# Performance work log

Measured on AMD Instinct MI355X. Metric: run time of the kernel, lower is better.

## Reference

```python
import jax, jax.numpy as jnp
import numpy as np

H = 64  # hidden size


def _lstm(hist, Wih, Whh, bih, bhh):
    # PyTorch single-layer LSTM, gate order [i, f, g, o]; hist: (T, in_dim)
    def step(carry, x):
        h, c = carry
        gates = Wih @ x + bih + Whh @ h + bhh  # (4H,)
        i, f, g, o = jnp.split(gates, 4)
        i, f, o = jax.nn.sigmoid(i), jax.nn.sigmoid(f), jax.nn.sigmoid(o)
        c = f * c + i * jnp.tanh(g)
        h = o * jnp.tanh(c)
        return (h, c), None
    h0 = jnp.zeros((H,), hist.dtype)
    (h, _), _ = jax.lax.scan(step, (h0, h0), hist)
    return h


def setup_inputs() -> dict:
    key = jax.random.key(0)
    ks = jax.random.split(key, 16)
    N, E, P, T = 100000, 3200000, 1000000, 200
    s = 0.05
    return {
        "node_feats": jax.random.normal(ks[0], (N, 2), jnp.float32),
        "edge_feats": jax.random.normal(ks[1], (E, 5), jnp.float32),
        "hist_tokens": jax.random.normal(ks[2], (T, 3), jnp.float32),
        "cand_pairs": jax.random.randint(ks[3], (P, 2), 0, N, jnp.int32),
        "N": N,
        "node_W": jax.random.normal(ks[4], (2, H), jnp.float32) * s,
        "node_b": jax.random.normal(ks[5], (H,), jnp.float32) * s,
        "edge_W": jax.random.normal(ks[6], (5, H), jnp.float32) * s,
        "edge_b": jax.random.normal(ks[7], (H,), jnp.float32) * s,
        "lstm_Wih": jax.random.normal(ks[8], (4 * H, 3), jnp.float32) * s,
        "lstm_Whh": jax.random.normal(ks[9], (4 * H, H), jnp.float32) * s,
        "lstm_bih": jax.random.normal(ks[10], (4 * H,), jnp.float32) * s,
        "lstm_bhh": jax.random.normal(ks[11], (4 * H,), jnp.float32) * s,
        "fuse_W1": jax.random.normal(ks[12], (3 * H + 2, H), jnp.float32) * s,
        "fuse_b1": jax.random.normal(ks[13], (H,), jnp.float32) * s,
        "fuse_W2": jax.random.normal(ks[14], (H, 1), jnp.float32) * s,
        "fuse_b2": jax.random.normal(ks[15], (1,), jnp.float32) * s,
    }


def reference(node_feats, edge_feats, hist_tokens, cand_pairs, N,
              node_W, node_b, edge_W, edge_b,
              lstm_Wih, lstm_Whh, lstm_bih, lstm_bhh,
              fuse_W1, fuse_b1, fuse_W2, fuse_b2):
    # encoder: mean-pooled node / edge MLPs -> (2H,)
    hn = jax.nn.relu(node_feats @ node_W + node_b).mean(0)
    he = jax.nn.relu(edge_feats @ edge_W + edge_b).mean(0)
    z_graph = jnp.concatenate([hn, he])  # (2H,)
    z_hist = _lstm(hist_tokens, lstm_Wih, lstm_Whh, lstm_bih, lstm_bhh)  # (H,)
    P = cand_pairs.shape[0]
    denom = jnp.float32(N - 1) + 1e-9
    cand = cand_pairs.astype(jnp.float32) / denom  # (P, 2)
    ctx = jnp.concatenate([z_graph, z_hist])  # (3H,)
    z = jnp.concatenate([jnp.broadcast_to(ctx, (P, 3 * H)), cand], axis=-1)  # (P, 3H+2)
    scores = jax.nn.relu(z @ fuse_W1 + fuse_b1) @ fuse_W2 + fuse_b2  # (P, 1)
    return scores[:, 0]
```

## Files before the change

kernel.cpp:

```cpp
#include <hip/hip_runtime.h>
#include <math.h>

#define H 64
#define WS_H 0
#define WS_FUSE 64
#define WS_PART 320
#define LOG2E 1.4426950408889634f

__device__ __forceinline__ float fast_sigmoid(float x) {
    float e = exp2f(-LOG2E * x);
    return __builtin_amdgcn_rcpf(1.f + e);
}
__device__ __forceinline__ float fast_tanh(float x) {
    x = fminf(fmaxf(x, -9.f), 9.f);
    float e = exp2f((2.f * LOG2E) * x);
    return (e - 1.f) * __builtin_amdgcn_rcpf(e + 1.f);
}

template<int K>
__device__ void encode_rows2(const float* __restrict__ X, const float* __restrict__ Wg,
                             const float* __restrict__ bias, int nrows,
                             int blk, int nblk, float* __restrict__ out, int tid)
{
    constexpr int TR = 512;
    __shared__ __align__(16) float xs[TR * K];
    int lane = tid & 63;
    int j0 = (tid >> 6) * 16;
    float w[K][16], bi[16], acc[16];
#pragma unroll
    for (int k = 0; k < K; ++k)
#pragma unroll
        for (int jj = 0; jj < 16; ++jj) w[k][jj] = Wg[k * H + j0 + jj];
#pragma unroll
    for (int jj = 0; jj < 16; ++jj) { bi[jj] = bias[j0 + jj]; acc[jj] = 0.f; }

    int ntiles = (nrows + TR - 1) / TR;
    for (int tile = blk; tile < ntiles; tile += nblk) {
        size_t base = (size_t)tile * TR;
        int cnt = nrows - (int)base; if (cnt > TR) cnt = TR;
        int ne = cnt * K;
        __syncthreads();
        const float* Xb = X + base * K;
        int n4 = ne >> 2;
        for (int idx = tid; idx < n4; idx += 256)
            ((float4*)xs)[idx] = ((const float4*)Xb)[idx];
        for (int idx = (n4 << 2) + tid; idx < ne; idx += 256)
            xs[idx] = Xb[idx];
        __syncthreads();
#pragma unroll
        for (int i = 0; i < TR / 64; ++i) {
            int r = i * 64 + lane;
            if (r < cnt) {
                float x[K];
#pragma unroll
                for (int k = 0; k < K; ++k) x[k] = xs[r * K + k];
#pragma unroll
                for (int jj = 0; jj < 16; ++jj) {
                    float t = bi[jj];
#pragma unroll
                    for (int k = 0; k < K; ++k) t = fmaf(x[k], w[k][jj], t);
                    acc[jj] += fmaxf(t, 0.f);
                }
            }
        }
    }
#pragma unroll
    for (int jj = 0; jj < 16; ++jj) {
        float v = acc[jj];
#pragma unroll
        for (int off = 32; off; off >>= 1) v += __shfl_xor(v, off);
        if (lane == jj) out[j0 + jj] = v;
    }
}

__global__ __launch_bounds__(256)
void k_encode_lstm(const float* __restrict__ node_feats,
                   const float* __restrict__ edge_feats,
                   const float* __restrict__ hist,
                   const float* __restrict__ node_W, const float* __restrict__ node_b,
                   const float* __restrict__ edge_W, const float* __restrict__ edge_b,
                   const float* __restrict__ Wih, const float* __restrict__ Whh,
                   const float* __restrict__ bih, const float* __restrict__ bhh,
                   int Nn, int Ne, int T, int eb, int nb,
                   float* __restrict__ ws)
{
    int tid = threadIdx.x;
    int b = blockIdx.x;

    if (b == 0) {
        __builtin_amdgcn_s_setprio(1);
        __shared__ float hcop[4][H];
        __shared__ __align__(16) float4 actx[2][H];
        __shared__ float hist_s[640];
        int w = tid >> 6, j = tid & 63;
        int row = tid;
        float whh[H];
#pragma unroll
        for (int k = 0; k < H; k += 4) {
            float4 v = *(const float4*)(Whh + row * H + k);
            whh[k] = v.x; whh[k+1] = v.y; whh[k+2] = v.z; whh[k+3] = v.w;
        }
        float wih0 = Wih[row*3+0], wih1 = Wih[row*3+1], wih2 = Wih[row*3+2];
        float bsum = bih[row] + bhh[row];
        for (int idx = tid; idx < T * 3; idx += 256) hist_s[idx] = hist[idx];
        hcop[w][j] = 0.f;
        float c = 0.f, h = 0.f;
        __syncthreads();

        for (int t = 0; t < T; ++t) {
            float x0 = hist_s[3*t], x1 = hist_s[3*t+1], x2 = hist_s[3*t+2];
            float g = fmaf(wih0, x0, fmaf(wih1, x1, fmaf(wih2, x2, bsum)));
            float a0 = 0.f, a1 = 0.f, a2 = 0.f, a3 = 0.f;
            const float4* hv = (const float4*)hcop[w];
#pragma unroll
            for (int k4 = 0; k4 < H / 4; ++k4) {
                float4 hh = hv[k4];
                a0 = fmaf(whh[4*k4+0], hh.x, a0);
                a1 = fmaf(whh[4*k4+1], hh.y, a1);
                a2 = fmaf(whh[4*k4+2], hh.z, a2);
                a3 = fmaf(whh[4*k4+3], hh.w, a3);
            }
            g += (a0 + a1) + (a2 + a3);
            float av = (w == 2) ? fast_tanh(g) : fast_sigmoid(g);
            ((float*)&actx[t & 1][j])[w] = av;
            __syncthreads();
            float4 a = actx[t & 1][j];
            c = fmaf(a.y, c, a.x * a.z);
            h = a.w * fast_tanh(c);
            hcop[w][j] = h;
        }
        if (w == 0) ws[WS_H + j] = h;
    } else if (b <= eb) {
        encode_rows2<5>(edge_feats, edge_W, edge_b, Ne, b - 1, eb,
                        ws + WS_PART + (size_t)(b - 1) * H, tid);
    } else {
        encode_rows2<2>(node_feats, node_W, node_b, Nn, b - 1 - eb, nb,
                        ws + WS_PART + (size_t)(eb + (b - 1 - eb)) * H, tid);
    }
}

__global__ __launch_bounds__(1024)
void k_finalize(const float* __restrict__ W1, const float* __restrict__ b1,
                const float* __restrict__ W2,
                float inv_n, float inv_e, float inv_denom,
                int eb, int nb, float* __restrict__ ws)
{
    int tid = threadIdx.x;
    int j = tid & 63, q = tid >> 6;
    __shared__ float tmpe[16][H], tmpn[16][H];
    __shared__ float ctx[3 * H];
    __shared__ float pt[16][H];

    float se = 0.f;
    for (int b = q; b < eb; b += 16) se += ws[WS_PART + (size_t)b * H + j];
    tmpe[q][j] = se;
    float sn = 0.f;
    for (int b = q; b < nb; b += 16) sn += ws[WS_PART + (size_t)(eb + b) * H + j];
    tmpn[q][j] = sn;
    __syncthreads();

    if (tid < H) {
        float s1 = 0.f, s2 = 0.f;
#pragma unroll
        for (int r = 0; r < 16; ++r) { s1 += tmpn[r][tid]; s2 += tmpe[r][tid]; }
        ctx[tid]         = s1 * inv_n;
        ctx[H + tid]     = s2 * inv_e;
        ctx[2 * H + tid] = ws[WS_H + tid];
    }
    __syncthreads();

    float p = 0.f;
#pragma unroll
    for (int kk = 0; kk < 12; ++kk) {
        int k = q * 12 + kk;
        p = fmaf(ctx[k], W1[(size_t)k * H + j], p);
    }
    pt[q][j] = p;
    __syncthreads();

    if (tid < H) {
        float bse = b1[tid];
#pragma unroll
        for (int r = 0; r < 16; ++r) bse += pt[r][tid];
        float4 v;
        v.x = bse;
        v.y = W1[(size_t)192 * H + tid] * inv_denom;
        v.z = W1[(size_t)193 * H + tid] * inv_denom;
        v.w = W2[tid];
        ((float4*)(ws + WS_FUSE))[tid] = v;
    }
}

__global__ __launch_bounds__(256)
void k_fuse(const int* __restrict__ pairs, const float* __restrict__ fb2,
            const float* __restrict__ ws, float* __restrict__ out, int P)
{
    __shared__ __align__(16) float4 sf[H];
    int tid = threadIdx.x;
    if (tid < H) sf[tid] = ((const float4*)(ws + WS_FUSE))[tid];
    __syncthreads();

    int i0 = blockIdx.x * 1024 + tid;
    float bias = fb2[0];
    float p0[4], p1[4], s[4];
#pragma unroll
    for (int q = 0; q < 4; ++q) {
        int i = i0 + q * 256;
        int2 pr = (i < P) ? ((const int2*)pairs)[i] : make_int2(0, 0);
        p0[q] = (float)pr.x; p1[q] = (float)pr.y; s[q] = bias;
    }
#pragma unroll
    for (int j = 0; j < H; ++j) {
        float4 v = sf[j];
#pragma unroll
        for (int q = 0; q < 4; ++q) {
            float hh = fmaf(p1[q], v.z, fmaf(p0[q], v.y, v.x));
            s[q] = fmaf(fmaxf(hh, 0.f), v.w, s[q]);
        }
    }
#pragma unroll
    for (int q = 0; q < 4; ++q) {
        int i = i0 + q * 256;
        if (i < P) out[i] = s[q];
    }
}

extern "C" void kernel_launch(void* const* d_in, const int* in_sizes, int n_in,
                              void* d_out, int out_size, void* d_ws, size_t ws_size,
                              hipStream_t stream) {
    const float* node_feats = (const float*)d_in[0];
    const float* edge_feats = (const float*)d_in[1];
    const float* hist       = (const float*)d_in[2];
    const int*   pairs      = (const int*)d_in[3];
    const float* node_W = (const float*)d_in[5];
    const float* node_b = (const float*)d_in[6];
    const float* edge_W = (const float*)d_in[7];
    const float* edge_b = (const float*)d_in[8];
    const float* Wih    = (const float*)d_in[9];
    const float* Whh    = (const float*)d_in[10];
    const float* bih    = (const float*)d_in[11];
    const float* bhh    = (const float*)d_in[12];
    const float* W1     = (const float*)d_in[13];
    const float* b1     = (const float*)d_in[14];
    const float* W2     = (const float*)d_in[15];
    const float* b2     = (const float*)d_in[16];

    int Nn = in_sizes[0] / 2;
    int Ne = in_sizes[1] / 5;
    int T  = in_sizes[2] / 3;
    int P  = in_sizes[3] / 2;

    int eb = 1024, nb = 64;
    while ((size_t)(WS_PART + (eb + nb) * H) * sizeof(float) > ws_size && eb > 8) {
        eb >>= 1; if (nb > 4) nb >>= 1;
    }

    float inv_n = (float)(1.0 / (double)Nn);
    float inv_e = (float)(1.0 / (double)Ne);
    float denomf = (float)(Nn - 1) + 1e-9f;
    float inv_denom = 1.0f / denomf;

    float* ws = (float*)d_ws;

    k_encode_lstm<<<1 + eb + nb, 256, 0, stream>>>(
        node_feats, edge_feats, hist, node_W, node_b, edge_W, edge_b,
        Wih, Whh, bih, bhh, Nn, Ne, T, eb, nb, ws);

    k_finalize<<<1, 1024, 0, stream>>>(W1, b1, W2, inv_n, inv_e, inv_denom, eb, nb, ws);

    int blocksC = (P + 1023) / 1024;
    k_fuse<<<blocksC, 256, 0, stream>>>(pairs, b2, ws, (float*)d_out, P);
}
```

Measured before the change: 144.5 us.

## Fuse finalize into encoder via last-block atomic and restructure LSTM recurrence

```diff
diff --git a/kernel.cpp b/kernel.cpp
--- a/kernel.cpp
+++ b/kernel.cpp
@@ -4,7 +4,8 @@
 #define H 64
 #define WS_H 0
 #define WS_FUSE 64
-#define WS_PART 320
+#define WS_CNT 320
+#define WS_PART 384
 #define LOG2E 1.4426950408889634f
 
 __device__ __forceinline__ float fast_sigmoid(float x) {
@@ -20,10 +21,10 @@
 template<int K>
 __device__ void encode_rows2(const float* __restrict__ X, const float* __restrict__ Wg,
                              const float* __restrict__ bias, int nrows,
-                             int blk, int nblk, float* __restrict__ out, int tid)
+                             int blk, int nblk, float* __restrict__ out, int tid,
+                             float* __restrict__ xs)
 {
     constexpr int TR = 512;
-    __shared__ __align__(16) float xs[TR * K];
     int lane = tid & 63;
     int j0 = (tid >> 6) * 16;
     float w[K][16], bi[16], acc[16];
@@ -73,96 +74,29 @@
     }
 }
 
-__global__ __launch_bounds__(256)
-void k_encode_lstm(const float* __restrict__ node_feats,
-                   const float* __restrict__ edge_feats,
-                   const float* __restrict__ hist,
-                   const float* __restrict__ node_W, const float* __restrict__ node_b,
-                   const float* __restrict__ edge_W, const float* __restrict__ edge_b,
-                   const float* __restrict__ Wih, const float* __restrict__ Whh,
-                   const float* __restrict__ bih, const float* __restrict__ bhh,
-                   int Nn, int Ne, int T, int eb, int nb,
-                   float* __restrict__ ws)
+__device__ void finalize_dev(int tid, const float* __restrict__ W1,
+                             const float* __restrict__ b1, const float* __restrict__ W2,
+                             float inv_n, float inv_e, float inv_denom,
+                             int eb, int nb, float* __restrict__ ws, float* __restrict__ fin)
 {
-    int tid = threadIdx.x;
-    int b = blockIdx.x;
-
-    if (b == 0) {
-        __builtin_amdgcn_s_setprio(1);
-        __shared__ float hcop[4][H];
-        __shared__ __align__(16) float4 actx[2][H];
-        __shared__ float hist_s[640];
-        int w = tid >> 6, j = tid & 63;
-        int row = tid;
-        float whh[H];
-#pragma unroll
-        for (int k = 0; k < H; k += 4) {
-            float4 v = *(const float4*)(Whh + row * H + k);
-            whh[k] = v.x; whh[k+1] = v.y; whh[k+2] = v.z; whh[k+3] = v.w;
-        }
-        float wih0 = Wih[row*3+0], wih1 = Wih[row*3+1], wih2 = Wih[row*3+2];
-        float bsum = bih[row] + bhh[row];
-        for (int idx = tid; idx < T * 3; idx += 256) hist_s[idx] = hist[idx];
-        hcop[w][j] = 0.f;
-        float c = 0.f, h = 0.f;
-        __syncthreads();
-
-        for (int t = 0; t < T; ++t) {
-            float x0 = hist_s[3*t], x1 = hist_s[3*t+1], x2 = hist_s[3*t+2];
-            float g = fmaf(wih0, x0, fmaf(wih1, x1, fmaf(wih2, x2, bsum)));
-            float a0 = 0.f, a1 = 0.f, a2 = 0.f, a3 = 0.f;
-            const float4* hv = (const float4*)hcop[w];
-#pragma unroll
-            for (int k4 = 0; k4 < H / 4; ++k4) {
-                float4 hh = hv[k4];
-                a0 = fmaf(whh[4*k4+0], hh.x, a0);
-                a1 = fmaf(whh[4*k4+1], hh.y, a1);
-                a2 = fmaf(whh[4*k4+2], hh.z, a2);
-                a3 = fmaf(whh[4*k4+3], hh.w, a3);
-            }
-            g += (a0 + a1) + (a2 + a3);
-            float av = (w == 2) ? fast_tanh(g) : fast_sigmoid(g);
-            ((float*)&actx[t & 1][j])[w] = av;
-            __syncthreads();
-            float4 a = actx[t & 1][j];
-            c = fmaf(a.y, c, a.x * a.z);
-            h = a.w * fast_tanh(c);
-            hcop[w][j] = h;
-        }
-        if (w == 0) ws[WS_H + j] = h;
-    } else if (b <= eb) {
-        encode_rows2<5>(edge_feats, edge_W, edge_b, Ne, b - 1, eb,
-                        ws + WS_PART + (size_t)(b - 1) * H, tid);
-    } else {
-        encode_rows2<2>(node_feats, node_W, node_b, Nn, b - 1 - eb, nb,
-                        ws + WS_PART + (size_t)(eb + (b - 1 - eb)) * H, tid);
-    }
-}
-
-__global__ __launch_bounds__(1024)
-void k_finalize(const float* __restrict__ W1, const float* __restrict__ b1,
-                const float* __restrict__ W2,
-                float inv_n, float inv_e, float inv_denom,
-                int eb, int nb, float* __restrict__ ws)
-{
-    int tid = threadIdx.x;
-    int j = tid & 63, q = tid >> 6;
-    __shared__ float tmpe[16][H], tmpn[16][H];
-    __shared__ float ctx[3 * H];
-    __shared__ float pt[16][H];
+    float* tmpe = fin;
+    float* tmpn = fin + 256;
+    float* ctx  = fin + 512;
+    float* pt   = fin + 704;
+    int q = tid >> 6, j = tid & 63;
+    const float* wsp = ws + WS_PART;
 
     float se = 0.f;
-    for (int b = q; b < eb; b += 16) se += ws[WS_PART + (size_t)b * H + j];
-    tmpe[q][j] = se;
+    for (int b = q; b < eb; b += 4) se += wsp[(size_t)b * H + j];
+    tmpe[q * H + j] = se;
     float sn = 0.f;
-    for (int b = q; b < nb; b += 16) sn += ws[WS_PART + (size_t)(eb + b) * H + j];
-    tmpn[q][j] = sn;
+    for (int b = q; b < nb; b += 4) sn += wsp[(size_t)(eb + b) * H + j];
+    tmpn[q * H + j] = sn;
     __syncthreads();
 
     if (tid < H) {
-        float s1 = 0.f, s2 = 0.f;
-#pragma unroll
-        for (int r = 0; r < 16; ++r) { s1 += tmpn[r][tid]; s2 += tmpe[r][tid]; }
+        float s1 = (tmpn[tid] + tmpn[H + tid]) + (tmpn[2 * H + tid] + tmpn[3 * H + tid]);
+        float s2 = (tmpe[tid] + tmpe[H + tid]) + (tmpe[2 * H + tid] + tmpe[3 * H + tid]);
         ctx[tid]         = s1 * inv_n;
         ctx[H + tid]     = s2 * inv_e;
         ctx[2 * H + tid] = ws[WS_H + tid];
@@ -171,23 +105,125 @@
 
     float p = 0.f;
 #pragma unroll
-    for (int kk = 0; kk < 12; ++kk) {
-        int k = q * 12 + kk;
+    for (int kk = 0; kk < 48; ++kk) {
+        int k = q * 48 + kk;
         p = fmaf(ctx[k], W1[(size_t)k * H + j], p);
     }
-    pt[q][j] = p;
+    pt[q * H + j] = p;
     __syncthreads();
 
     if (tid < H) {
-        float bse = b1[tid];
-#pragma unroll
-        for (int r = 0; r < 16; ++r) bse += pt[r][tid];
+        float bse = b1[tid] + (pt[tid] + pt[H + tid]) + (pt[2 * H + tid] + pt[3 * H + tid]);
         float4 v;
         v.x = bse;
         v.y = W1[(size_t)192 * H + tid] * inv_denom;
         v.z = W1[(size_t)193 * H + tid] * inv_denom;
         v.w = W2[tid];
         ((float4*)(ws + WS_FUSE))[tid] = v;
+    }
+}
+
+__global__ __launch_bounds__(256)
+void k_main(const float* __restrict__ node_feats, const float* __restrict__ edge_feats,
+            const float* __restrict__ hist,
+            const float* __restrict__ node_W, const float* __restrict__ node_b,
+            const float* __restrict__ edge_W, const float* __restrict__ edge_b,
+            const float* __restrict__ Wih, const float* __restrict__ Whh,
+            const float* __restrict__ bih, const float* __restrict__ bhh,
+            const float* __restrict__ W1, const float* __restrict__ b1,
+            const float* __restrict__ W2,
+            float inv_n, float inv_e, float inv_denom,
+            int Nn, int Ne, int T, int eb, int nb,
+            float* __restrict__ ws)
+{
+    __shared__ __align__(16) char smem[12800];
+    __shared__ unsigned lastflag;
+    int tid = threadIdx.x;
+    int b = blockIdx.x;
+
+    if (b == 0) {
+        float* pb     = (float*)smem;
+        float* hist_f = (float*)(smem + 10240);
+        int s = tid >> 6, j = tid & 63;
+        int kbase = __builtin_amdgcn_readfirstlane((tid >> 6) << 4);
+
+        float w[4][16];
+#pragma unroll
+        for (int g = 0; g < 4; ++g) {
+            const float* wr = Whh + (size_t)(g * H + j) * H + kbase;
+#pragma unroll
+            for (int m4 = 0; m4 < 4; ++m4) {
+                float4 v = *(const float4*)(wr + 4 * m4);
+                w[g][4*m4+0] = v.x; w[g][4*m4+1] = v.y; w[g][4*m4+2] = v.z; w[g][4*m4+3] = v.w;
+            }
+        }
+        float wi0[4], wi1[4], wi2[4], bb[4];
+#pragma unroll
+        for (int g = 0; g < 4; ++g) {
+            int row = g * H + j;
+            wi0[g] = Wih[row*3+0]; wi1[g] = Wih[row*3+1]; wi2[g] = Wih[row*3+2];
+            bb[g] = bih[row] + bhh[row];
+        }
+        for (int idx = tid; idx < T * 3; idx += 256) hist_f[idx] = hist[idx];
+        float hs[16];
+#pragma unroll
+        for (int m = 0; m < 16; ++m) hs[m] = 0.f;
+        float c = 0.f, h = 0.f;
+        __syncthreads();
+        float x0 = hist_f[0], x1 = hist_f[1], x2 = hist_f[2];
+        __builtin_amdgcn_s_setprio(1);
+
+        for (int t = 0; t < T; ++t) {
+            float a0 = 0.f, a1 = 0.f, a2 = 0.f, a3 = 0.f;
+#pragma unroll
+            for (int m = 0; m < 16; ++m) {
+                a0 = fmaf(w[0][m], hs[m], a0);
+                a1 = fmaf(w[1][m], hs[m], a1);
+                a2 = fmaf(w[2][m], hs[m], a2);
+                a3 = fmaf(w[3][m], hs[m], a3);
+            }
+            float xb0 = fmaf(wi2[0], x2, fmaf(wi1[0], x1, fmaf(wi0[0], x0, bb[0])));
+            float xb1 = fmaf(wi2[1], x2, fmaf(wi1[1], x1, fmaf(wi0[1], x0, bb[1])));
+            float xb2 = fmaf(wi2[2], x2, fmaf(wi1[2], x1, fmaf(wi0[2], x0, bb[2])));
+            float xb3 = fmaf(wi2[3], x2, fmaf(wi1[3], x1, fmaf(wi0[3], x0, bb[3])));
+            float4 part; part.x = a0; part.y = a1; part.z = a2; part.w = a3;
+            *(float4*)(pb + ((size_t)((t & 1) * 64 + j)) * 20 + 4 * s) = part;
+            if (t + 1 < T) { x0 = hist_f[3*t+3]; x1 = hist_f[3*t+4]; x2 = hist_f[3*t+5]; }
+            __syncthreads();
+            const float* row = pb + ((size_t)((t & 1) * 64 + j)) * 20;
+            float4 p0 = *(const float4*)(row + 0);
+            float4 p1 = *(const float4*)(row + 4);
+            float4 p2 = *(const float4*)(row + 8);
+            float4 p3 = *(const float4*)(row + 12);
+            float gi = fast_sigmoid((p0.x + p1.x) + (p2.x + p3.x) + xb0);
+            float gf = fast_sigmoid((p0.y + p1.y) + (p2.y + p3.y) + xb1);
+            float gg = fast_tanh  ((p0.z + p1.z) + (p2.z + p3.z) + xb2);
+            float go = fast_sigmoid((p0.w + p1.w) + (p2.w + p3.w) + xb3);
+            c = fmaf(gf, c, gi * gg);
+            h = go * fast_tanh(c);
+#pragma unroll
+            for (int m = 0; m < 16; ++m)
+                hs[m] = __int_as_float(__builtin_amdgcn_readlane(__float_as_int(h), kbase + m));
+        }
+        __builtin_amdgcn_s_setprio(0);
+        if (s == 0) ws[WS_H + j] = h;
+    } else if (b <= eb) {
+        encode_rows2<5>(edge_feats, edge_W, edge_b, Ne, b - 1, eb,
+                        ws + WS_PART + (size_t)(b - 1) * H, tid, (float*)smem);
+    } else {
+        encode_rows2<2>(node_feats, node_W, node_b, Nn, b - 1 - eb, nb,
+                        ws + WS_PART + (size_t)(eb + (b - 1 - eb)) * H, tid, (float*)smem);
+    }
+
+    __threadfence();
+    if (tid == 0) {
+        unsigned prev = atomicAdd((unsigned*)(ws + WS_CNT), 1u);
+        lastflag = (prev == (unsigned)(gridDim.x - 1)) ? 1u : 0u;
+    }
+    __syncthreads();
+    if (lastflag) {
+        __threadfence();
+        finalize_dev(tid, W1, b1, W2, inv_n, inv_e, inv_denom, eb, nb, ws, (float*)smem);
     }
 }
 
@@ -200,28 +236,28 @@
     if (tid < H) sf[tid] = ((const float4*)(ws + WS_FUSE))[tid];
     __syncthreads();
 
-    int i0 = blockIdx.x * 1024 + tid;
+    int i0 = blockIdx.x * 2048 + tid;
     float bias = fb2[0];
-    float p0[4], p1[4], s[4];
-#pragma unroll
-    for (int q = 0; q < 4; ++q) {
+    float p0[8], p1[8], sc[8];
+#pragma unroll
+    for (int q = 0; q < 8; ++q) {
         int i = i0 + q * 256;
         int2 pr = (i < P) ? ((const int2*)pairs)[i] : make_int2(0, 0);
-        p0[q] = (float)pr.x; p1[q] = (float)pr.y; s[q] = bias;
-    }
-#pragma unroll
-    for (int j = 0; j < H; ++j) {
-        float4 v = sf[j];
-#pragma unroll
-        for (int q = 0; q < 4; ++q) {
+        p0[q] = (float)pr.x; p1[q] = (float)pr.y; sc[q] = bias;
+    }
+#pragma unroll
+    for (int jj = 0; jj < H; ++jj) {
+        float4 v = sf[jj];
+#pragma unroll
+        for (int q = 0; q < 8; ++q) {
             float hh = fmaf(p1[q], v.z, fmaf(p0[q], v.y, v.x));
-            s[q] = fmaf(fmaxf(hh, 0.f), v.w, s[q]);
-        }
-    }
-#pragma unroll
-    for (int q = 0; q < 4; ++q) {
+            sc[q] = fmaf(fmaxf(hh, 0.f), v.w, sc[q]);
+        }
+    }
+#pragma unroll
+    for (int q = 0; q < 8; ++q) {
         int i = i0 + q * 256;
-        if (i < P) out[i] = s[q];
+        if (i < P) out[i] = sc[q];
     }
 }
 
@@ -262,12 +298,13 @@
 
     float* ws = (float*)d_ws;
 
-    k_encode_lstm<<<1 + eb + nb, 256, 0, stream>>>(
+    hipMemsetAsync((char*)d_ws + WS_CNT * sizeof(float), 0, sizeof(unsigned), stream);
+
+    k_main<<<1 + eb + nb, 256, 0, stream>>>(
         node_feats, edge_feats, hist, node_W, node_b, edge_W, edge_b,
-        Wih, Whh, bih, bhh, Nn, Ne, T, eb, nb, ws);
-
-    k_finalize<<<1, 1024, 0, stream>>>(W1, b1, W2, inv_n, inv_e, inv_denom, eb, nb, ws);
-
-    int blocksC = (P + 1023) / 1024;
+        Wih, Whh, bih, bhh, W1, b1, W2,
+        inv_n, inv_e, inv_denom, Nn, Ne, T, eb, nb, ws);
+
+    int blocksC = (P + 2047) / 2048;
     k_fuse<<<blocksC, 256, 0, stream>>>(pairs, b2, ws, (float*)d_out, P);
 }
```

After: 230.7 us. +59.7%, slower.
